# Kernel tuning notes

Measured on AMD Instinct MI355X. Metric: run time of the kernel, lower is better.

The kernel has to match this reference:

```python
import jax, jax.numpy as jnp
import numpy as np

N = 8192        # batch_size == num nodes == num hyperedges
D = 512         # hidden_dim
H_HEADS = 8
HD = D // H_HEADS
TOP_K = 16
EPS = 1e-5      # LayerNorm eps


def setup_inputs() -> dict:
    key = jax.random.key(0)
    ks = jax.random.split(key, 10)
    def rn(k, shape, scale=0.02):
        return jax.random.normal(k, shape, dtype=jnp.float32) * scale
    return {
        "x0": jax.random.normal(ks[0], (N, D), dtype=jnp.float32),
        "x1": jax.random.normal(ks[1], (N, D), dtype=jnp.float32),
        # modality projections: Linear -> ReLU -> LayerNorm (per modality)
        "w_p0": rn(ks[2], (D, D)), "b_p0": jnp.zeros((D,), jnp.float32),
        "g0": jnp.ones((D,), jnp.float32), "beta0": jnp.zeros((D,), jnp.float32),
        "w_p1": rn(ks[3], (D, D)), "b_p1": jnp.zeros((D,), jnp.float32),
        "g1": jnp.ones((D,), jnp.float32), "beta1": jnp.zeros((D,), jnp.float32),
        # MultiheadAttention packed in-proj + out-proj
        "in_w": rn(ks[4], (3 * D, D)), "in_b": jnp.zeros((3 * D,), jnp.float32),
        "out_w": rn(ks[5], (D, D)), "out_b": jnp.zeros((D,), jnp.float32),
        # edge weight predictor MLP
        "ew_w1": rn(ks[6], (D // 2, D)), "ew_b1": jnp.zeros((D // 2,), jnp.float32),
        "ew_w2": rn(ks[7], (1, D // 2)), "ew_b2": jnp.zeros((1,), jnp.float32),
    }


def _layernorm(x, g, b):
    m = x.mean(-1, keepdims=True)
    v = ((x - m) ** 2).mean(-1, keepdims=True)
    return (x - m) * jax.lax.rsqrt(v + EPS) * g + b


def _forward(x0, x1, w_p0, b_p0, g0, beta0, w_p1, b_p1, g1, beta1,
             in_w, in_b, out_w, out_b, ew_w1, ew_b1, ew_w2, ew_b2):
    # per-modality projection: Linear -> ReLU -> LayerNorm
    p0 = _layernorm(jax.nn.relu(x0 @ w_p0.T + b_p0), g0, beta0)
    p1 = _layernorm(jax.nn.relu(x1 @ w_p1.T + b_p1), g1, beta1)
    seq = jnp.stack([p0, p1], axis=1)                       # [N, 2, D]
    # cross-modal MHA (self-attention over the 2 modality tokens)
    qkv = seq @ in_w.T + in_b                               # [N, 2, 3D]
    q, k, v = jnp.split(qkv, 3, axis=-1)
    q = q.reshape(N, 2, H_HEADS, HD)
    k = k.reshape(N, 2, H_HEADS, HD)
    v = v.reshape(N, 2, H_HEADS, HD)
    scores = jnp.einsum('bqhd,bkhd->bhqk', q, k) / jnp.sqrt(jnp.float32(HD))
    attn = jax.nn.softmax(scores, axis=-1)                  # [N, h, 2, 2]
    ctx = jnp.einsum('bhqk,bkhd->bqhd', attn, v).reshape(N, 2, D)
    attended = ctx @ out_w.T + out_b                        # [N, 2, D]
    fused = attended.mean(axis=1)                           # [N, D]
    # node-node attention similarity, row-softmax
    sim = jax.nn.softmax(fused @ fused.T, axis=1)           # [N, N]
    _, idx = jax.lax.top_k(sim, TOP_K)                      # [N, K]
    vals = jnp.take_along_axis(sim, idx, axis=1)            # [N, K]
    rows = jnp.arange(N)
    # H[i,i]=1 first, then H[neighbor, i] = sim[i, neighbor] (may overwrite diag)
    H = jnp.zeros((N, N), sim.dtype).at[rows, rows].set(1.0)
    H = H.at[idx, rows[:, None]].set(vals)
    colsum = H.sum(axis=0)
    H = H.at[rows, rows].set(jnp.where(colsum == 0, 1.0, H[rows, rows]))
    # edge weights
    hidden = jax.nn.relu(fused @ ew_w1.T + ew_b1)
    ew = jax.nn.sigmoid(hidden @ ew_w2.T + ew_b2)[:, 0]     # [N]
    ew = jnp.maximum(ew, 1e-8)
    return H, ew


def reference(x0, x1, w_p0, b_p0, g0, beta0, w_p1, b_p1, g1, beta1,
              in_w, in_b, out_w, out_b, ew_w1, ew_b1, ew_w2, ew_b2):
    return _forward(x0, x1, w_p0, b_p0, g0, beta0, w_p1, b_p1, g1, beta1,
                    in_w, in_b, out_w, out_b, ew_w1, ew_b1, ew_w2, ew_b2)
```

## Files before the change

kernel.cpp:

```cpp
#include <hip/hip_runtime.h>
#include <hip/hip_bf16.h>

#define NN 8192
#define DD 512

typedef unsigned short u16;
typedef __bf16 bf16_t;
typedef bf16_t bf16x8 __attribute__((ext_vector_type(8)));
typedef float f32x4 __attribute__((ext_vector_type(4)));

__device__ __forceinline__ float bf2f(u16 h) {
    union { unsigned u; float f; } v; v.u = ((unsigned)h) << 16; return v.f;
}
__device__ __forceinline__ float bflo(unsigned u) {
    union { unsigned u; float f; } v; v.u = u << 16; return v.f;
}
__device__ __forceinline__ float bfhi(unsigned u) {
    union { unsigned u; float f; } v; v.u = u & 0xFFFF0000u; return v.f;
}
__device__ __forceinline__ u16 f2bf(float f) {
    union { float f; unsigned u; } v; v.f = f;
    unsigned r = v.u + 0x7fffu + ((v.u >> 16) & 1u);
    return (u16)(r >> 16);
}

__global__ __launch_bounds__(256) void cvt7(
        const float* __restrict__ s0, u16* __restrict__ d0,
        const float* __restrict__ s1, u16* __restrict__ d1,
        const float* __restrict__ s2, u16* __restrict__ d2,
        const float* __restrict__ s3, u16* __restrict__ d3,
        const float* __restrict__ s4, u16* __restrict__ d4,
        const float* __restrict__ s5, u16* __restrict__ d5,
        const float* __restrict__ s6, u16* __restrict__ d6) {
    size_t v = ((size_t)blockIdx.x * 256 + threadIdx.x) * 8;
    const float* s; u16* d; size_t off;
    if (v < 4194304)      { s = s0; d = d0; off = v; }
    else if (v < 8388608) { s = s1; d = d1; off = v - 4194304; }
    else if (v < 8650752) { s = s2; d = d2; off = v - 8388608; }
    else if (v < 8912896) { s = s3; d = d3; off = v - 8650752; }
    else if (v < 9699328) { s = s4; d = d4; off = v - 8912896; }
    else if (v < 9961472) { s = s5; d = d5; off = v - 9699328; }
    else                  { s = s6; d = d6; off = v - 9961472; }
    float4 a = *(const float4*)(s + off);
    float4 b = *(const float4*)(s + off + 4);
    ushort4 o0 = make_ushort4(f2bf(a.x), f2bf(a.y), f2bf(a.z), f2bf(a.w));
    ushort4 o1 = make_ushort4(f2bf(b.x), f2bf(b.y), f2bf(b.z), f2bf(b.w));
    *(ushort4*)(d + off) = o0;
    *(ushort4*)(d + off + 4) = o1;
}

#define EPS_LDS 136
template<bool RELU, bool BIAS, bool SPLIT>
__global__ __launch_bounds__(256) void gemm_bt(const u16* __restrict__ A,
        const u16* __restrict__ B, const float* __restrict__ bias,
        const u16* __restrict__ B2, const float* __restrict__ bias2, int halfY,
        u16* __restrict__ C, int M, int Nc, int K) {
    __shared__ alignas(16) u16 Smem[2][16384];
    const int t = threadIdx.x;
    const int lane = t & 63;
    const int wave = t >> 6;
    const int wm = (wave >> 1) * 64;
    const int wn = (wave & 1) * 64;
    const int rowA = blockIdx.y * 128;
    const int rowB = blockIdx.x * 128;
    if (SPLIT && (int)blockIdx.y >= halfY) { B = B2; bias = bias2; }

    f32x4 acc[4][4] = {};
    const int mrow = lane & 15;
    const int kk = (lane >> 4) * 8;
    const int nt = K >> 6;

    auto STAGE = [&](int buf, int k0) {
        u16* As = Smem[buf];
        u16* Bs = Smem[buf] + 8192;
        #pragma unroll
        for (int r = 0; r < 4; ++r) {
            int chunk = r * 256 + t;
            const u16* srcA = A + (size_t)(rowA + (chunk >> 3)) * K + k0 + (chunk & 7) * 8;
            __builtin_amdgcn_global_load_lds(
                (const __attribute__((address_space(1))) void*)srcA,
                (__attribute__((address_space(3))) void*)(As + chunk * 8), 16, 0, 0);
            const u16* srcB = B + (size_t)(rowB + (chunk >> 3)) * K + k0 + (chunk & 7) * 8;
            __builtin_amdgcn_global_load_lds(
                (const __attribute__((address_space(1))) void*)srcB,
                (__attribute__((address_space(3))) void*)(Bs + chunk * 8), 16, 0, 0);
        }
    };

    STAGE(0, 0);
    __syncthreads();
    int cur = 0;
    for (int ti = 0; ti < nt; ++ti) {
        if (ti + 1 < nt) STAGE(cur ^ 1, (ti + 1) << 6);
        const u16* As = Smem[cur];
        const u16* Bs = Smem[cur] + 8192;
        #pragma unroll
        for (int ks = 0; ks < 64; ks += 32) {
            bf16x8 af[4], bfv[4];
            #pragma unroll
            for (int i = 0; i < 4; ++i)
                af[i] = *(const bf16x8*)(As + (wm + i * 16 + mrow) * 64 + ks + kk);
            #pragma unroll
            for (int j = 0; j < 4; ++j)
                bfv[j] = *(const bf16x8*)(Bs + (wn + j * 16 + mrow) * 64 + ks + kk);
            #pragma unroll
            for (int i = 0; i < 4; ++i)
                #pragma unroll
                for (int j = 0; j < 4; ++j)
                    acc[i][j] = __builtin_amdgcn_mfma_f32_16x16x32_bf16(af[i], bfv[j], acc[i][j], 0, 0, 0);
        }
        __syncthreads();
        cur ^= 1;
    }

    u16* Ep = &Smem[0][0];
    const int er0 = wm + (lane >> 4) * 4;
    const int ec0 = wn + (lane & 15);
    #pragma unroll
    for (int j = 0; j < 4; ++j) {
        int c = ec0 + j * 16;
        float bv = BIAS ? bias[rowB + c] : 0.0f;
        #pragma unroll
        for (int i = 0; i < 4; ++i) {
            #pragma unroll
            for (int r = 0; r < 4; ++r) {
                float v = acc[i][j][r] + bv;
                if (RELU) v = fmaxf(v, 0.0f);
                Ep[(er0 + i * 16 + r) * EPS_LDS + c] = f2bf(v);
            }
        }
    }
    __syncthreads();
    #pragma unroll
    for (int pass = 0; pass < 8; ++pass) {
        int chunk = pass * 256 + t;
        int rloc = chunk >> 4, coff = (chunk & 15) * 8;
        bf16x8 v = *(const bf16x8*)(Ep + rloc * EPS_LDS + coff);
        *(bf16x8*)(C + (size_t)(rowA + rloc) * Nc + rowB + coff) = v;
    }
}

__global__ __launch_bounds__(256) void gemm_qkv(const u16* __restrict__ A,
        const u16* __restrict__ B, const float* __restrict__ bias,
        u16* __restrict__ V, float* __restrict__ scores) {
    __shared__ alignas(16) u16 Smem[2][16384];
    const int t = threadIdx.x;
    const int lane = t & 63;
    const int wave = t >> 6;
    const int wm = (wave >> 1) * 64;
    const int wn = (wave & 1) * 64;
    const int c = blockIdx.x;
    const int rowA = blockIdx.y * 128;
    const bool isQK = (c < 8);

    f32x4 acc[4][4] = {};
    const int mrow = lane & 15;
    const int kk = (lane >> 4) * 8;

    auto STAGE = [&](int buf, int k0) {
        u16* As = Smem[buf];
        u16* Bs = Smem[buf] + 8192;
        #pragma unroll
        for (int r = 0; r < 4; ++r) {
            int chunk = r * 256 + t;
            int rr = chunk >> 3;
            int brow = isQK ? (c * 64 + rr + ((rr >= 64) ? 448 : 0))
                            : (1024 + (c - 8) * 128 + rr);
            const u16* srcA = A + (size_t)(rowA + rr) * DD + k0 + (chunk & 7) * 8;
            __builtin_amdgcn_global_load_lds(
                (const __attribute__((address_space(1))) void*)srcA,
                (__attribute__((address_space(3))) void*)(As + chunk * 8), 16, 0, 0);
            const u16* srcB = B + (size_t)brow * DD + k0 + (chunk & 7) * 8;
            __builtin_amdgcn_global_load_lds(
                (const __attribute__((address_space(1))) void*)srcB,
                (__attribute__((address_space(3))) void*)(Bs + chunk * 8), 16, 0, 0);
        }
    };

    STAGE(0, 0);
    __syncthreads();
    int cur = 0;
    for (int ti = 0; ti < 8; ++ti) {
        if (ti + 1 < 8) STAGE(cur ^ 1, (ti + 1) << 6);
        const u16* As = Smem[cur];
        const u16* Bs = Smem[cur] + 8192;
        #pragma unroll
        for (int ks = 0; ks < 64; ks += 32) {
            bf16x8 af[4], bfv[4];
            #pragma unroll
            for (int i = 0; i < 4; ++i)
                af[i] = *(const bf16x8*)(As + (wm + i * 16 + mrow) * 64 + ks + kk);
            #pragma unroll
            for (int j = 0; j < 4; ++j)
                bfv[j] = *(const bf16x8*)(Bs + (wn + j * 16 + mrow) * 64 + ks + kk);
            #pragma unroll
            for (int i = 0; i < 4; ++i)
                #pragma unroll
                for (int j = 0; j < 4; ++j)
                    acc[i][j] = __builtin_amdgcn_mfma_f32_16x16x32_bf16(af[i], bfv[j], acc[i][j], 0, 0, 0);
        }
        __syncthreads();
        cur ^= 1;
    }

    u16* Ep = &Smem[0][0];
    const int er0 = wm + (lane >> 4) * 4;
    const int ec0 = wn + (lane & 15);
    #pragma unroll
    for (int j = 0; j < 4; ++j) {
        int cc = ec0 + j * 16;
        int bcol = isQK ? ((cc < 64) ? c * 64 + cc : 448 + c * 64 + cc)
                        : (1024 + (c - 8) * 128 + cc);
        float bv = bias[bcol];
        #pragma unroll
        for (int i = 0; i < 4; ++i) {
            #pragma unroll
            for (int r = 0; r < 4; ++r)
                Ep[(er0 + i * 16 + r) * EPS_LDS + cc] = f2bf(acc[i][j][r] + bv);
        }
    }
    __syncthreads();
    if (isQK) {
        int nd = t >> 2, cb = t & 3, tt2 = cb >> 1, ss = cb & 1;
        const u16* qrow = Ep + (2 * nd + tt2) * EPS_LDS;
        const u16* krow = Ep + (2 * nd + ss) * EPS_LDS + 64;
        float s = 0.0f;
        #pragma unroll
        for (int d8 = 0; d8 < 8; ++d8) {
            bf16x8 qv = *(const bf16x8*)(qrow + d8 * 8);
            bf16x8 kv = *(const bf16x8*)(krow + d8 * 8);
            #pragma unroll
            for (int u = 0; u < 8; ++u) s += (float)qv[u] * (float)kv[u];
        }
        scores[(size_t)(rowA / 2 + nd) * 32 + c * 4 + cb] = s * 0.125f;
    } else {
        #pragma unroll
        for (int pass = 0; pass < 8; ++pass) {
            int chunk = pass * 256 + t;
            int rloc = chunk >> 4, coff = (chunk & 15) * 8;
            bf16x8 v = *(const bf16x8*)(Ep + rloc * EPS_LDS + coff);
            *(bf16x8*)(V + (size_t)(rowA + rloc) * 512 + (c - 8) * 128 + coff) = v;
        }
    }
}

#define SYM_LDS 129
__global__ __launch_bounds__(256) void gemm_symh(const u16* __restrict__ F,
        u16* __restrict__ C, const u16* __restrict__ W1,
        const float* __restrict__ b1, u16* __restrict__ Hid) {
    __shared__ alignas(16) u16 Smem[2][16384];
    const int bx = blockIdx.x, by = blockIdx.y;
    const bool isHid = (bx >= 64);
    if (!isHid && bx < by) return;
    const int t = threadIdx.x;
    const int lane = t & 63;
    const int wave = t >> 6;
    const int wm = (wave >> 1) * 64;
    const int wn = (wave & 1) * 64;
    const int rowI = by * 128;
    const int rowJ = isHid ? (bx - 64) * 128 : bx * 128;
    const u16* Bsrc = isHid ? W1 : F;

    f32x4 acc[4][4] = {};
    const int mrow = lane & 15;
    const int kk = (lane >> 4) * 8;

    auto STAGE = [&](int buf, int k0) {
        u16* As = Smem[buf];
        u16* Bs = Smem[buf] + 8192;
        #pragma unroll
        for (int r = 0; r < 4; ++r) {
            int chunk = r * 256 + t;
            const u16* srcA = F + (size_t)(rowI + (chunk >> 3)) * DD + k0 + (chunk & 7) * 8;
            __builtin_amdgcn_global_load_lds(
                (const __attribute__((address_space(1))) void*)srcA,
                (__attribute__((address_space(3))) void*)(As + chunk * 8), 16, 0, 0);
            const u16* srcB = Bsrc + (size_t)(rowJ + (chunk >> 3)) * DD + k0 + (chunk & 7) * 8;
            __builtin_amdgcn_global_load_lds(
                (const __attribute__((address_space(1))) void*)srcB,
                (__attribute__((address_space(3))) void*)(Bs + chunk * 8), 16, 0, 0);
        }
    };

    STAGE(0, 0);
    __syncthreads();
    int cur = 0;
    for (int ti = 0; ti < 8; ++ti) {
        if (ti + 1 < 8) STAGE(cur ^ 1, (ti + 1) << 6);
        const u16* As = Smem[cur];
        const u16* Bs = Smem[cur] + 8192;
        #pragma unroll
        for (int ks = 0; ks < 64; ks += 32) {
            bf16x8 af[4], bfv[4];
            #pragma unroll
            for (int i = 0; i < 4; ++i)
                af[i] = *(const bf16x8*)(As + (wm + i * 16 + mrow) * 64 + ks + kk);
            #pragma unroll
            for (int j = 0; j < 4; ++j)
                bfv[j] = *(const bf16x8*)(Bs + (wn + j * 16 + mrow) * 64 + ks + kk);
            #pragma unroll
            for (int i = 0; i < 4; ++i)
                #pragma unroll
                for (int j = 0; j < 4; ++j)
                    acc[i][j] = __builtin_amdgcn_mfma_f32_16x16x32_bf16(af[i], bfv[j], acc[i][j], 0, 0, 0);
        }
        __syncthreads();
        cur ^= 1;
    }

    u16* Ep = &Smem[0][0];
    const int er0 = wm + (lane >> 4) * 4;
    const int ec0 = wn + (lane & 15);
    #pragma unroll
    for (int j = 0; j < 4; ++j) {
        int c = ec0 + j * 16;
        float bv = isHid ? b1[rowJ + c] : 0.0f;
        #pragma unroll
        for (int i = 0; i < 4; ++i) {
            #pragma unroll
            for (int r = 0; r < 4; ++r) {
                float v = acc[i][j][r] + bv;
                if (isHid) v = fmaxf(v, 0.0f);
                Ep[(er0 + i * 16 + r) * SYM_LDS + c] = f2bf(v);
            }
        }
    }
    __syncthreads();
    if (isHid) {
        #pragma unroll
        for (int pass = 0; pass < 8; ++pass) {
            int chunk = pass * 256 + t;
            int rloc = chunk >> 4, coff = (chunk & 15) * 8;
            union { u16 us[8]; bf16x8 v; } buf;
            #pragma unroll
            for (int k = 0; k < 8; ++k) buf.us[k] = Ep[rloc * SYM_LDS + coff + k];
            *(bf16x8*)(Hid + (size_t)(rowI + rloc) * 256 + rowJ + coff) = buf.v;
        }
        return;
    }
    #pragma unroll
    for (int pass = 0; pass < 8; ++pass) {
        int chunk = pass * 256 + t;
        int rloc = chunk >> 4, coff = (chunk & 15) * 8;
        union { u16 us[8]; bf16x8 v; } buf;
        #pragma unroll
        for (int k = 0; k < 8; ++k) buf.us[k] = Ep[rloc * SYM_LDS + coff + k];
        *(bf16x8*)(C + (size_t)(rowI + rloc) * NN + rowJ + coff) = buf.v;
    }
    if (bx != by) {
        #pragma unroll
        for (int pass = 0; pass < 8; ++pass) {
            int chunk = pass * 256 + t;
            int tr = chunk >> 4, roff = (chunk & 15) * 8;
            union { u16 us[8]; bf16x8 v; } buf;
            #pragma unroll
            for (int k = 0; k < 8; ++k) buf.us[k] = Ep[(roff + k) * SYM_LDS + tr];
            *(bf16x8*)(C + (size_t)(rowJ + tr) * NN + rowI + roff) = buf.v;
        }
    }
}

__global__ __launch_bounds__(256) void ln2_kernel(const u16* __restrict__ y,
        const float* __restrict__ g0, const float* __restrict__ b0,
        const float* __restrict__ g1, const float* __restrict__ b1,
        u16* __restrict__ seq) {
    int n = blockIdx.x * 4 + (threadIdx.x >> 6);
    int lane = threadIdx.x & 63;
    int modality = n >> 13, node = n & (NN - 1);
    const float* g = modality ? g1 : g0;
    const float* b = modality ? b1 : b0;
    bf16x8 v = *(const bf16x8*)(y + (size_t)n * DD + lane * 8);
    float x[8];
    float s = 0.0f;
    #pragma unroll
    for (int u = 0; u < 8; ++u) { x[u] = (float)v[u]; s += x[u]; }
    #pragma unroll
    for (int off = 32; off; off >>= 1) s += __shfl_xor(s, off);
    float mean = s * (1.0f / DD);
    float vs = 0.0f;
    #pragma unroll
    for (int u = 0; u < 8; ++u) { x[u] -= mean; vs += x[u] * x[u]; }
    #pragma unroll
    for (int off = 32; off; off >>= 1) vs += __shfl_xor(vs, off);
    float inv = rsqrtf(vs * (1.0f / DD) + 1e-5f);
    float4 ga = *(const float4*)(g + lane * 8);
    float4 gb = *(const float4*)(g + lane * 8 + 4);
    float4 ba = *(const float4*)(b + lane * 8);
    float4 bb = *(const float4*)(b + lane * 8 + 4);
    union { u16 us[8]; bf16x8 v; } o;
    o.us[0] = f2bf(x[0] * inv * ga.x + ba.x);
    o.us[1] = f2bf(x[1] * inv * ga.y + ba.y);
    o.us[2] = f2bf(x[2] * inv * ga.z + ba.z);
    o.us[3] = f2bf(x[3] * inv * ga.w + ba.w);
    o.us[4] = f2bf(x[4] * inv * gb.x + bb.x);
    o.us[5] = f2bf(x[5] * inv * gb.y + bb.y);
    o.us[6] = f2bf(x[6] * inv * gb.z + bb.z);
    o.us[7] = f2bf(x[7] * inv * gb.w + bb.w);
    *(bf16x8*)(seq + (size_t)node * (2 * DD) + modality * DD + lane * 8) = o.v;
}

__global__ __launch_bounds__(256) void attn_v(const float* __restrict__ scores,
        const u16* __restrict__ V, u16* __restrict__ ctxm) {
    int n = blockIdx.x * 4 + (threadIdx.x >> 6);
    int lane = threadIdx.x & 63;
    int h = lane >> 3;
    float4 sc = *(const float4*)(scores + (size_t)n * 32 + h * 4);
    float s00 = sc.x, s01 = sc.y, s10 = sc.z, s11 = sc.w;
    float m0 = fmaxf(s00, s01), e00 = __expf(s00 - m0), e01 = __expf(s01 - m0);
    float a00 = e00 / (e00 + e01), a01 = e01 / (e00 + e01);
    float m1 = fmaxf(s10, s11), e10 = __expf(s10 - m1), e11 = __expf(s11 - m1);
    float a10 = e10 / (e10 + e11), a11 = e11 / (e10 + e11);
    float al0 = 0.5f * (a00 + a10), al1 = 0.5f * (a01 + a11);
    bf16x8 v0 = *(const bf16x8*)(V + (size_t)(2 * n) * 512 + lane * 8);
    bf16x8 v1 = *(const bf16x8*)(V + (size_t)(2 * n + 1) * 512 + lane * 8);
    union { u16 us[8]; bf16x8 v; } o;
    #pragma unroll
    for (int u = 0; u < 8; ++u)
        o.us[u] = f2bf(al0 * (float)v0[u] + al1 * (float)v1[u]);
    *(bf16x8*)(ctxm + (size_t)n * 512 + lane * 8) = o.v;
}

__global__ __launch_bounds__(256) void topk_bf16(u16* __restrict__ S,
        float* __restrict__ topv, int* __restrict__ topi,
        u16* __restrict__ hidden, const float* __restrict__ w2,
        const float* __restrict__ b2, float* __restrict__ ew_out,
        float* __restrict__ H) {
    const int blk = blockIdx.x;
    const int t = threadIdx.x;
    const float4 z4 = make_float4(0.f, 0.f, 0.f, 0.f);
    if (blk >= 2048) {
        int wv = t >> 6, lane = t & 63;
        int n0 = (blk - 2048) * 64 + wv * 16;
        float wa = w2[lane], wb = w2[lane + 64], wc = w2[lane + 128], wd = w2[lane + 192];
        for (int q = 0; q < 16; ++q) {
            int n = n0 + q;
            const u16* hr = hidden + (size_t)n * 256;
            float s = bf2f(hr[lane]) * wa + bf2f(hr[lane + 64]) * wb
                    + bf2f(hr[lane + 128]) * wc + bf2f(hr[lane + 192]) * wd;
            #pragma unroll
            for (int off = 32; off; off >>= 1) s += __shfl_xor(s, off);
            if (lane == 0) {
                float z = s + b2[0];
                float sig = 1.0f / (1.0f + __expf(-z));
                ew_out[n] = fmaxf(sig, 1e-8f);
            }
        }
        float4* zb = (float4*)(hidden + (size_t)n0 * 256);
        #pragma unroll
        for (int i = 0; i < 8; ++i) zb[i * 64 + lane] = z4;
        return;
    }
    const float NEG = -3e38f;
    const int SENT = 0x7FFFFFFF;
    int row = blk * 4 + (t >> 6);
    int lane = t & 63;
    u16* Sr = S + (size_t)row * NN;

    float m = NEG, l = 0.0f;
    float t1v = NEG, t2v = NEG, t3v = NEG;
    int t1i = SENT, t2i = SENT, t3i = SENT;

    #pragma unroll
    for (int p = 0; p < 16; ++p) {
        uint4 raw = *(const uint4*)(Sr + p * 512 + lane * 8);
        int base = p * 512 + lane * 8;
        #pragma unroll
        for (int q = 0; q < 4; ++q) {
            unsigned w = (&raw.x)[q];
            #pragma unroll
            for (int h = 0; h < 2; ++h) {
                float x = h ? bfhi(w) : bflo(w);
                int xi = base + q * 2 + h;
                if (x > m) { l = l * __expf(m - x) + 1.0f; m = x; }
                else l += __expf(x - m);
                bool g1 = x > t1v, g2 = x > t2v, g3 = x > t3v;
                t3v = g2 ? t2v : (g3 ? x : t3v);
                t3i = g2 ? t2i : (g3 ? xi : t3i);
                t2v = g1 ? t1v : (g2 ? x : t2v);
                t2i = g1 ? t1i : (g2 ? xi : t2i);
                t1v = g1 ? x : t1v;
                t1i = g1 ? xi : t1i;
            }
        }
    }
    #pragma unroll
    for (int off = 32; off; off >>= 1) {
        float om = __shfl_xor(m, off);
        float ol = __shfl_xor(l, off);
        float nm = fmaxf(m, om);
        l = l * __expf(m - nm) + ol * __expf(om - nm);
        m = nm;
    }

    unsigned mk0 = 0, mk1 = 0, mk2 = 0, mk3 = 0;
    float c1v = t1v, c2v = t2v, c3v = t3v;
    int c1i = t1i, c2i = t2i, c3i = t3i;
    for (int r = 0; r < 16; ++r) {
        float wv = c1v; int wi = c1i;
        #pragma unroll
        for (int off = 32; off; off >>= 1) {
            float ov = __shfl_xor(wv, off);
            int oi = __shfl_xor(wi, off);
            if (ov > wv || (ov == wv && oi < wi)) { wv = ov; wi = oi; }
        }
        if (lane == 0) {
            topv[(size_t)row * 16 + r] = __expf(wv - m) / l;
            topi[(size_t)row * 16 + r] = wi;
        }
        if (wi == c1i) {
            int slot = ((wi >> 9) << 3) | (wi & 7);
            unsigned bit = 1u << (slot & 31);
            if (slot < 32) mk0 |= bit; else if (slot < 64) mk1 |= bit;
            else if (slot < 96) mk2 |= bit; else mk3 |= bit;
            c1v = c2v; c1i = c2i;
            c2v = c3v; c2i = c3i;
            c3v = NEG; c3i = SENT;
            if (c1i == SENT) {
                float nb = NEG; int ni = SENT;
                #pragma unroll
                for (int p = 0; p < 16; ++p) {
                    uint4 raw = *(const uint4*)(Sr + p * 512 + lane * 8);
                    int base = p * 512 + lane * 8;
                    #pragma unroll
                    for (int q = 0; q < 4; ++q) {
                        unsigned w = (&raw.x)[q];
                        #pragma unroll
                        for (int h = 0; h < 2; ++h) {
                            int sl = p * 8 + q * 2 + h;
                            unsigned mw = (sl < 32) ? mk0 : (sl < 64) ? mk1
                                        : (sl < 96) ? mk2 : mk3;
                            float x = ((mw >> (sl & 31)) & 1u) ? NEG
                                    : (h ? bfhi(w) : bflo(w));
                            if (x > nb) { nb = x; ni = base + q * 2 + h; }
                        }
                    }
                }
                c1v = nb; c1i = ni;
            }
        }
    }

    float4* srow = (float4*)Sr;
    #pragma unroll
    for (int i = 0; i < 16; ++i) srow[i * 64 + lane] = z4;

    {
        size_t vb0 = (size_t)blk * 63488;
        #pragma unroll
        for (int rr = 0; rr < 16; ++rr) {
            int j = rr * 256 + t;
            if (j < 3968) {
                size_t b = vb0 + (size_t)j * 16;
                char* p = (char*)H + (b < 109051904u ? b : b + 4194304u);
                *(float4*)p = z4;
            }
        }
    }
}

__global__ __launch_bounds__(256) void scatter_diag(const float* __restrict__ topv,
        const int* __restrict__ topi, float* __restrict__ H) {
    int tk = blockIdx.x * 256 + threadIdx.x;
    if (tk < NN * 16) {
        int i = tk >> 4;
        int idx = topi[tk];
        H[(size_t)idx * NN + i] = topv[tk];
    } else {
        int c = tk - NN * 16;
        const int* ti = topi + c * 16;
        bool self = false;
        #pragma unroll
        for (int j = 0; j < 16; ++j) self |= (ti[j] == c);
        if (!self) H[(size_t)c * NN + c] = 1.0f;
    }
}

extern "C" void kernel_launch(void* const* d_in, const int* in_sizes, int n_in,
                              void* d_out, int out_size, void* d_ws, size_t ws_size,
                              hipStream_t stream) {
    const float* x0    = (const float*)d_in[0];
    const float* x1    = (const float*)d_in[1];
    const float* w_p0  = (const float*)d_in[2];
    const float* b_p0  = (const float*)d_in[3];
    const float* g0    = (const float*)d_in[4];
    const float* beta0 = (const float*)d_in[5];
    const float* w_p1  = (const float*)d_in[6];
    const float* b_p1  = (const float*)d_in[7];
    const float* g1    = (const float*)d_in[8];
    const float* beta1 = (const float*)d_in[9];
    const float* in_w  = (const float*)d_in[10];
    const float* in_b  = (const float*)d_in[11];
    const float* out_w = (const float*)d_in[12];
    const float* out_b = (const float*)d_in[13];
    const float* ew_w1 = (const float*)d_in[14];
    const float* ew_b1 = (const float*)d_in[15];
    const float* ew_w2 = (const float*)d_in[16];
    const float* ew_b2 = (const float*)d_in[17];

    float* Hf = (float*)d_out;
    float* ew_out = Hf + (size_t)NN * NN;

    u16* Hu = (u16*)d_out;
    u16* x0b    = Hu;
    u16* x1b    = Hu + 4194304;
    u16* y01    = Hu + 8388608;
    u16* seq    = Hu + 16777216;
    u16* Vbuf   = Hu + 25165824;
    u16* ctxm   = Hu + 50331648;
    u16* hidden = Hu + 54525952;
    float* scB  = (float*)(Hu + 58720256);
    u16* wp0b   = Hu + 60817408;
    u16* wp1b   = wp0b + 262144;
    u16* inwb   = wp1b + 262144;
    u16* outwb  = inwb + 786432;
    u16* eww1b  = outwb + 262144;
    u16* Sb     = Hu + 67108864;
    char* ws = (char*)d_ws;
    u16* fusedB = (u16*)ws;
    float* topv = (float*)(ws + (8u << 20));
    int*   topi = (int*)(ws + (8u << 20) + 524288);

    dim3 blk(256);
    const int BIG = 1 << 30;
    cvt7<<<dim3(4928), blk, 0, stream>>>(x0, x0b, x1, x1b, w_p0, wp0b, w_p1, wp1b,
                                         in_w, inwb, out_w, outwb, ew_w1, eww1b);
    gemm_bt<true, true, true><<<dim3(4, 128), blk, 0, stream>>>(
        x0b, wp0b, b_p0, wp1b, b_p1, 64, y01, 2 * NN, DD, DD);
    ln2_kernel<<<dim3(2 * NN / 4), blk, 0, stream>>>(y01, g0, beta0, g1, beta1, seq);
    gemm_qkv<<<dim3(12, 128), blk, 0, stream>>>(seq, inwb, in_b, Vbuf, scB);
    attn_v<<<dim3(NN / 4), blk, 0, stream>>>(scB, Vbuf, ctxm);
    gemm_bt<false, true, false><<<dim3(4, 64), blk, 0, stream>>>(
        ctxm, outwb, out_b, nullptr, nullptr, BIG, fusedB, NN, DD, DD);
    gemm_symh<<<dim3(66, 64), blk, 0, stream>>>(fusedB, Sb, eww1b, ew_b1, hidden);
    topk_bf16<<<dim3(2176), blk, 0, stream>>>(Sb, topv, topi,
        hidden, ew_w2, ew_b2, ew_out, Hf);
    scatter_diag<<<dim3((NN * 16 + NN) / 256), blk, 0, stream>>>(topv, topi, Hf);
}
```

Measured before the change: 570.4 us.

## Fuse input bf16 conversion, attention softmax and context mix into GEMM prologues

The projection GEMM now loads fp32 inputs directly and converts them to bf16 in registers before writing to LDS, removing the separate conversion pass over x0/x1. The QKV GEMM epilogue computes the two-token softmax and mean attention weights via lane shuffles and stores only the per-head averaged weights. The out-projection GEMM builds its A operand on the fly from V and those weights, removing the attn_v kernel and the ctx buffer round-trip. This saves several full-size memory passes and two launches, at the cost of register-staged A loads that bypass the async global-to-LDS path.

```diff
diff --git a/kernel.cpp b/kernel.cpp
--- a/kernel.cpp
+++ b/kernel.cpp
@@ -24,23 +24,19 @@
     return (u16)(r >> 16);
 }
 
-__global__ __launch_bounds__(256) void cvt7(
+__global__ __launch_bounds__(256) void cvt5(
         const float* __restrict__ s0, u16* __restrict__ d0,
         const float* __restrict__ s1, u16* __restrict__ d1,
         const float* __restrict__ s2, u16* __restrict__ d2,
         const float* __restrict__ s3, u16* __restrict__ d3,
-        const float* __restrict__ s4, u16* __restrict__ d4,
-        const float* __restrict__ s5, u16* __restrict__ d5,
-        const float* __restrict__ s6, u16* __restrict__ d6) {
+        const float* __restrict__ s4, u16* __restrict__ d4) {
     size_t v = ((size_t)blockIdx.x * 256 + threadIdx.x) * 8;
     const float* s; u16* d; size_t off;
-    if (v < 4194304)      { s = s0; d = d0; off = v; }
-    else if (v < 8388608) { s = s1; d = d1; off = v - 4194304; }
-    else if (v < 8650752) { s = s2; d = d2; off = v - 8388608; }
-    else if (v < 8912896) { s = s3; d = d3; off = v - 8650752; }
-    else if (v < 9699328) { s = s4; d = d4; off = v - 8912896; }
-    else if (v < 9961472) { s = s5; d = d5; off = v - 9699328; }
-    else                  { s = s6; d = d6; off = v - 9961472; }
+    if (v < 262144)       { s = s0; d = d0; off = v; }
+    else if (v < 524288)  { s = s1; d = d1; off = v - 262144; }
+    else if (v < 1310720) { s = s2; d = d2; off = v - 524288; }
+    else if (v < 1572864) { s = s3; d = d3; off = v - 1310720; }
+    else                  { s = s4; d = d4; off = v - 1572864; }
     float4 a = *(const float4*)(s + off);
     float4 b = *(const float4*)(s + off + 4);
     ushort4 o0 = make_ushort4(f2bf(a.x), f2bf(a.y), f2bf(a.z), f2bf(a.w));
@@ -50,11 +46,11 @@
 }
 
 #define EPS_LDS 136
-template<bool RELU, bool BIAS, bool SPLIT>
-__global__ __launch_bounds__(256) void gemm_bt(const u16* __restrict__ A,
-        const u16* __restrict__ B, const float* __restrict__ bias,
-        const u16* __restrict__ B2, const float* __restrict__ bias2, int halfY,
-        u16* __restrict__ C, int M, int Nc, int K) {
+__global__ __launch_bounds__(256) void gemm_proj(
+        const float* __restrict__ X0, const float* __restrict__ X1,
+        const u16* __restrict__ B0, const float* __restrict__ bias0,
+        const u16* __restrict__ B1, const float* __restrict__ bias1,
+        u16* __restrict__ C) {
     __shared__ alignas(16) u16 Smem[2][16384];
     const int t = threadIdx.x;
     const int lane = t & 63;
@@ -63,35 +59,59 @@
     const int wn = (wave & 1) * 64;
     const int rowA = blockIdx.y * 128;
     const int rowB = blockIdx.x * 128;
-    if (SPLIT && (int)blockIdx.y >= halfY) { B = B2; bias = bias2; }
+    const bool mod1 = (int)blockIdx.y >= 64;
+    const float* A32 = mod1 ? X1 + (size_t)(rowA - 8192) * DD
+                            : X0 + (size_t)rowA * DD;
+    const u16* B = mod1 ? B1 : B0;
+    const float* bias = mod1 ? bias1 : bias0;
 
     f32x4 acc[4][4] = {};
     const int mrow = lane & 15;
     const int kk = (lane >> 4) * 8;
-    const int nt = K >> 6;
-
-    auto STAGE = [&](int buf, int k0) {
+    const int trow = t >> 3;
+    const int koff = (t & 7) * 8;
+
+    float ar[4][8];
+    auto LOADA = [&](int k0) {
+        #pragma unroll
+        for (int r = 0; r < 4; ++r) {
+            const float* s = A32 + (size_t)(r * 32 + trow) * DD + k0 + koff;
+            float4 f0 = *(const float4*)s;
+            float4 f1 = *(const float4*)(s + 4);
+            ar[r][0] = f0.x; ar[r][1] = f0.y; ar[r][2] = f0.z; ar[r][3] = f0.w;
+            ar[r][4] = f1.x; ar[r][5] = f1.y; ar[r][6] = f1.z; ar[r][7] = f1.w;
+        }
+    };
+    auto WRITEA = [&](int buf) {
         u16* As = Smem[buf];
-        u16* Bs = Smem[buf] + 8192;
         #pragma unroll
         for (int r = 0; r < 4; ++r) {
             int chunk = r * 256 + t;
-            const u16* srcA = A + (size_t)(rowA + (chunk >> 3)) * K + k0 + (chunk & 7) * 8;
-            __builtin_amdgcn_global_load_lds(
-                (const __attribute__((address_space(1))) void*)srcA,
-                (__attribute__((address_space(3))) void*)(As + chunk * 8), 16, 0, 0);
-            const u16* srcB = B + (size_t)(rowB + (chunk >> 3)) * K + k0 + (chunk & 7) * 8;
+            ushort4 o0 = make_ushort4(f2bf(ar[r][0]), f2bf(ar[r][1]),
+                                      f2bf(ar[r][2]), f2bf(ar[r][3]));
+            ushort4 o1 = make_ushort4(f2bf(ar[r][4]), f2bf(ar[r][5]),
+                                      f2bf(ar[r][6]), f2bf(ar[r][7]));
+            *(ushort4*)(As + chunk * 8) = o0;
+            *(ushort4*)(As + chunk * 8 + 4) = o1;
+        }
+    };
+    auto BSTAGE = [&](int buf, int k0) {
+        u16* Bs = Smem[buf] + 8192;
+        #pragma unroll
+        for (int r = 0; r < 4; ++r) {
+            int chunk = r * 256 + t;
+            const u16* srcB = B + (size_t)(rowB + (chunk >> 3)) * DD + k0 + (chunk & 7) * 8;
             __builtin_amdgcn_global_load_lds(
                 (const __attribute__((address_space(1))) void*)srcB,
                 (__attribute__((address_space(3))) void*)(Bs + chunk * 8), 16, 0, 0);
         }
     };
 
-    STAGE(0, 0);
+    LOADA(0); BSTAGE(0, 0); WRITEA(0);
     __syncthreads();
     int cur = 0;
-    for (int ti = 0; ti < nt; ++ti) {
-        if (ti + 1 < nt) STAGE(cur ^ 1, (ti + 1) << 6);
+    for (int ti = 0; ti < 8; ++ti) {
+        if (ti < 7) { LOADA((ti + 1) << 6); BSTAGE(cur ^ 1, (ti + 1) << 6); }
         const u16* As = Smem[cur];
         const u16* Bs = Smem[cur] + 8192;
         #pragma unroll
@@ -109,6 +129,7 @@
                 for (int j = 0; j < 4; ++j)
                     acc[i][j] = __builtin_amdgcn_mfma_f32_16x16x32_bf16(af[i], bfv[j], acc[i][j], 0, 0, 0);
         }
+        if (ti < 7) WRITEA(cur ^ 1);
         __syncthreads();
         cur ^= 1;
     }
@@ -119,13 +140,12 @@
     #pragma unroll
     for (int j = 0; j < 4; ++j) {
         int c = ec0 + j * 16;
-        float bv = BIAS ? bias[rowB + c] : 0.0f;
+        float bv = bias[rowB + c];
         #pragma unroll
         for (int i = 0; i < 4; ++i) {
             #pragma unroll
             for (int r = 0; r < 4; ++r) {
-                float v = acc[i][j][r] + bv;
-                if (RELU) v = fmaxf(v, 0.0f);
+                float v = fmaxf(acc[i][j][r] + bv, 0.0f);
                 Ep[(er0 + i * 16 + r) * EPS_LDS + c] = f2bf(v);
             }
         }
@@ -136,13 +156,13 @@
         int chunk = pass * 256 + t;
         int rloc = chunk >> 4, coff = (chunk & 15) * 8;
         bf16x8 v = *(const bf16x8*)(Ep + rloc * EPS_LDS + coff);
-        *(bf16x8*)(C + (size_t)(rowA + rloc) * Nc + rowB + coff) = v;
+        *(bf16x8*)(C + (size_t)(rowA + rloc) * DD + rowB + coff) = v;
     }
 }
 
 __global__ __launch_bounds__(256) void gemm_qkv(const u16* __restrict__ A,
         const u16* __restrict__ B, const float* __restrict__ bias,
-        u16* __restrict__ V, float* __restrict__ scores) {
+        u16* __restrict__ V, float* __restrict__ AL) {
     __shared__ alignas(16) u16 Smem[2][16384];
     const int t = threadIdx.x;
     const int lane = t & 63;
@@ -232,7 +252,15 @@
             #pragma unroll
             for (int u = 0; u < 8; ++u) s += (float)qv[u] * (float)kv[u];
         }
-        scores[(size_t)(rowA / 2 + nd) * 32 + c * 4 + cb] = s * 0.125f;
+        s *= 0.125f;
+        float o = __shfl_xor(s, 1);
+        float mm = fmaxf(s, o);
+        float es = __expf(s - mm), eo = __expf(o - mm);
+        float a = es / (es + eo);
+        float a2 = __shfl_xor(a, 2);
+        float al = 0.5f * (a + a2);
+        if (cb < 2)
+            AL[(size_t)(rowA / 2 + nd) * 16 + c * 2 + cb] = al;
     } else {
         #pragma unroll
         for (int pass = 0; pass < 8; ++pass) {
@@ -241,6 +269,116 @@
             bf16x8 v = *(const bf16x8*)(Ep + rloc * EPS_LDS + coff);
             *(bf16x8*)(V + (size_t)(rowA + rloc) * 512 + (c - 8) * 128 + coff) = v;
         }
+    }
+}
+
+__global__ __launch_bounds__(256) void gemm_outp(
+        const float* __restrict__ AL, const u16* __restrict__ V,
+        const u16* __restrict__ W, const float* __restrict__ bias,
+        u16* __restrict__ C) {
+    __shared__ alignas(16) u16 Smem[2][16384];
+    const int t = threadIdx.x;
+    const int lane = t & 63;
+    const int wave = t >> 6;
+    const int wm = (wave >> 1) * 64;
+    const int wn = (wave & 1) * 64;
+    const int rowA = blockIdx.y * 128;
+    const int rowB = blockIdx.x * 128;
+
+    f32x4 acc[4][4] = {};
+    const int mrow = lane & 15;
+    const int kk = (lane >> 4) * 8;
+    const int trow = t >> 3;
+    const int koff = (t & 7) * 8;
+
+    uint4 v0r[4], v1r[4];
+    float2 alr[4];
+    auto LOADA = [&](int ti) {
+        #pragma unroll
+        for (int r = 0; r < 4; ++r) {
+            int node = rowA + r * 32 + trow;
+            alr[r] = *(const float2*)(AL + (size_t)node * 16 + ti * 2);
+            const u16* v0p = V + (size_t)(2 * node) * 512 + ti * 64 + koff;
+            v0r[r] = *(const uint4*)v0p;
+            v1r[r] = *(const uint4*)(v0p + 512);
+        }
+    };
+    auto WRITEA = [&](int buf) {
+        u16* As = Smem[buf];
+        #pragma unroll
+        for (int r = 0; r < 4; ++r) {
+            int chunk = r * 256 + t;
+            union { u16 us[8]; ushort4 u4[2]; } o;
+            #pragma unroll
+            for (int q = 0; q < 4; ++q) {
+                unsigned w0 = (&v0r[r].x)[q], w1 = (&v1r[r].x)[q];
+                o.us[q * 2]     = f2bf(alr[r].x * bflo(w0) + alr[r].y * bflo(w1));
+                o.us[q * 2 + 1] = f2bf(alr[r].x * bfhi(w0) + alr[r].y * bfhi(w1));
+            }
+            *(ushort4*)(As + chunk * 8) = o.u4[0];
+            *(ushort4*)(As + chunk * 8 + 4) = o.u4[1];
+        }
+    };
+    auto BSTAGE = [&](int buf, int k0) {
+        u16* Bs = Smem[buf] + 8192;
+        #pragma unroll
+        for (int r = 0; r < 4; ++r) {
+            int chunk = r * 256 + t;
+            const u16* srcB = W + (size_t)(rowB + (chunk >> 3)) * DD + k0 + (chunk & 7) * 8;
+            __builtin_amdgcn_global_load_lds(
+                (const __attribute__((address_space(1))) void*)srcB,
+                (__attribute__((address_space(3))) void*)(Bs + chunk * 8), 16, 0, 0);
+        }
+    };
+
+    LOADA(0); BSTAGE(0, 0); WRITEA(0);
+    __syncthreads();
+    int cur = 0;
+    for (int ti = 0; ti < 8; ++ti) {
+        if (ti < 7) { LOADA(ti + 1); BSTAGE(cur ^ 1, (ti + 1) << 6); }
+        const u16* As = Smem[cur];
+        const u16* Bs = Smem[cur] + 8192;
+        #pragma unroll
+        for (int ks = 0; ks < 64; ks += 32) {
+            bf16x8 af[4], bfv[4];
+            #pragma unroll
+            for (int i = 0; i < 4; ++i)
+                af[i] = *(const bf16x8*)(As + (wm + i * 16 + mrow) * 64 + ks + kk);
+            #pragma unroll
+            for (int j = 0; j < 4; ++j)
+                bfv[j] = *(const bf16x8*)(Bs + (wn + j * 16 + mrow) * 64 + ks + kk);
+            #pragma unroll
+            for (int i = 0; i < 4; ++i)
+                #pragma unroll
+                for (int j = 0; j < 4; ++j)
+                    acc[i][j] = __builtin_amdgcn_mfma_f32_16x16x32_bf16(af[i], bfv[j], acc[i][j], 0, 0, 0);
+        }
+        if (ti < 7) WRITEA(cur ^ 1);
+        __syncthreads();
+        cur ^= 1;
+    }
+
+    u16* Ep = &Smem[0][0];
+    const int er0 = wm + (lane >> 4) * 4;
+    const int ec0 = wn + (lane & 15);
+    #pragma unroll
+    for (int j = 0; j < 4; ++j) {
+        int c = ec0 + j * 16;
+        float bv = bias[rowB + c];
+        #pragma unroll
+        for (int i = 0; i < 4; ++i) {
+            #pragma unroll
+            for (int r = 0; r < 4; ++r)
+                Ep[(er0 + i * 16 + r) * EPS_LDS + c] = f2bf(acc[i][j][r] + bv);
+        }
+    }
+    __syncthreads();
+    #pragma unroll
+    for (int pass = 0; pass < 8; ++pass) {
+        int chunk = pass * 256 + t;
+        int rloc = chunk >> 4, coff = (chunk & 15) * 8;
+        bf16x8 v = *(const bf16x8*)(Ep + rloc * EPS_LDS + coff);
+        *(bf16x8*)(C + (size_t)(rowA + rloc) * DD + rowB + coff) = v;
     }
 }
 
@@ -397,27 +535,6 @@
     o.us[6] = f2bf(x[6] * inv * gb.z + bb.z);
     o.us[7] = f2bf(x[7] * inv * gb.w + bb.w);
     *(bf16x8*)(seq + (size_t)node * (2 * DD) + modality * DD + lane * 8) = o.v;
-}
-
-__global__ __launch_bounds__(256) void attn_v(const float* __restrict__ scores,
-        const u16* __restrict__ V, u16* __restrict__ ctxm) {
-    int n = blockIdx.x * 4 + (threadIdx.x >> 6);
-    int lane = threadIdx.x & 63;
-    int h = lane >> 3;
-    float4 sc = *(const float4*)(scores + (size_t)n * 32 + h * 4);
-    float s00 = sc.x, s01 = sc.y, s10 = sc.z, s11 = sc.w;
-    float m0 = fmaxf(s00, s01), e00 = __expf(s00 - m0), e01 = __expf(s01 - m0);
-    float a00 = e00 / (e00 + e01), a01 = e01 / (e00 + e01);
-    float m1 = fmaxf(s10, s11), e10 = __expf(s10 - m1), e11 = __expf(s11 - m1);
-    float a10 = e10 / (e10 + e11), a11 = e11 / (e10 + e11);
-    float al0 = 0.5f * (a00 + a10), al1 = 0.5f * (a01 + a11);
-    bf16x8 v0 = *(const bf16x8*)(V + (size_t)(2 * n) * 512 + lane * 8);
-    bf16x8 v1 = *(const bf16x8*)(V + (size_t)(2 * n + 1) * 512 + lane * 8);
-    union { u16 us[8]; bf16x8 v; } o;
-    #pragma unroll
-    for (int u = 0; u < 8; ++u)
-        o.us[u] = f2bf(al0 * (float)v0[u] + al1 * (float)v1[u]);
-    *(bf16x8*)(ctxm + (size_t)n * 512 + lane * 8) = o.v;
 }
 
 __global__ __launch_bounds__(256) void topk_bf16(u16* __restrict__ S,
@@ -601,14 +718,11 @@
     float* ew_out = Hf + (size_t)NN * NN;
 
     u16* Hu = (u16*)d_out;
-    u16* x0b    = Hu;
-    u16* x1b    = Hu + 4194304;
     u16* y01    = Hu + 8388608;
     u16* seq    = Hu + 16777216;
     u16* Vbuf   = Hu + 25165824;
-    u16* ctxm   = Hu + 50331648;
     u16* hidden = Hu + 54525952;
-    float* scB  = (float*)(Hu + 58720256);
+    float* ALb  = (float*)(Hu + 58720256);
     u16* wp0b   = Hu + 60817408;
     u16* wp1b   = wp0b + 262144;
     u16* inwb   = wp1b + 262144;
@@ -621,16 +735,13 @@
     int*   topi = (int*)(ws + (8u << 20) + 524288);
 
     dim3 blk(256);
-    const int BIG = 1 << 30;
-    cvt7<<<dim3(4928), blk, 0, stream>>>(x0, x0b, x1, x1b, w_p0, wp0b, w_p1, wp1b,
-                                         in_w, inwb, out_w, outwb, ew_w1, eww1b);
-    gemm_bt<true, true, true><<<dim3(4, 128), blk, 0, stream>>>(
-        x0b, wp0b, b_p0, wp1b, b_p1, 64, y01, 2 * NN, DD, DD);
+    cvt5<<<dim3(832), blk, 0, stream>>>(w_p0, wp0b, w_p1, wp1b,
+                                        in_w, inwb, out_w, outwb, ew_w1, eww1b);
+    gemm_proj<<<dim3(4, 128), blk, 0, stream>>>(
+        x0, x1, wp0b, b_p0, wp1b, b_p1, y01);
     ln2_kernel<<<dim3(2 * NN / 4), blk, 0, stream>>>(y01, g0, beta0, g1, beta1, seq);
-    gemm_qkv<<<dim3(12, 128), blk, 0, stream>>>(seq, inwb, in_b, Vbuf, scB);
-    attn_v<<<dim3(NN / 4), blk, 0, stream>>>(scB, Vbuf, ctxm);
-    gemm_bt<false, true, false><<<dim3(4, 64), blk, 0, stream>>>(
-        ctxm, outwb, out_b, nullptr, nullptr, BIG, fusedB, NN, DD, DD);
+    gemm_qkv<<<dim3(12, 128), blk, 0, stream>>>(seq, inwb, in_b, Vbuf, ALb);
+    gemm_outp<<<dim3(4, 64), blk, 0, stream>>>(ALb, Vbuf, outwb, out_b, fusedB);
     gemm_symh<<<dim3(66, 64), blk, 0, stream>>>(fusedB, Sb, eww1b, ew_b1, hidden);
     topk_bf16<<<dim3(2176), blk, 0, stream>>>(Sb, topv, topi,
         hidden, ew_w2, ew_b2, ew_out, Hf);
```

Result: slower. 596.3 us (+4.5%).
